# Kernel tuning notes

Measured on AMD Instinct MI355X. Metric: run time of the kernel, lower is better.

Reference implementation:

```python
import jax, jax.numpy as jnp
import numpy as np

N, E, D_IN, D, HEADS = 8192, 2048, 256, 256, 4
EPS = 1e-5
NEG = -1e9  # large negative instead of -inf (rows guaranteed non-empty anyway)


def _layernorm(x, g, b):
    mu = jnp.mean(x, axis=-1, keepdims=True)
    var = jnp.mean(jnp.square(x - mu), axis=-1, keepdims=True)
    return (x - mu) * jax.lax.rsqrt(var + EPS) * g + b


def _mha(q_x, kv_x, in_w, in_b, out_w, out_b, mask):
    """torch nn.MultiheadAttention (batch=1, eval) with boolean attn_mask.
    q_x: [Lq, D], kv_x: [Lk, D], mask: [Lq, Lk] True = blocked."""
    hd = D // HEADS
    wq, wk, wv = jnp.split(in_w, 3, axis=0)   # each [D, D]
    bq, bk, bv = jnp.split(in_b, 3, axis=0)
    q = (q_x @ wq.T + bq).reshape(-1, HEADS, hd).transpose(1, 0, 2)  # [h, Lq, hd]
    k = (kv_x @ wk.T + bk).reshape(-1, HEADS, hd).transpose(1, 0, 2)
    v = (kv_x @ wv.T + bv).reshape(-1, HEADS, hd).transpose(1, 0, 2)
    scores = jnp.einsum('hqd,hkd->hqk', q, k) / jnp.sqrt(jnp.asarray(hd, q.dtype))
    scores = jnp.where(mask[None, :, :], NEG, scores)
    attn = jax.nn.softmax(scores, axis=-1)
    out = jnp.einsum('hqk,hkd->hqd', attn, v)           # [h, Lq, hd]
    out = out.transpose(1, 0, 2).reshape(-1, D)          # [Lq, D]
    return out @ out_w.T + out_b


def setup_inputs() -> dict:
    key = jax.random.key(0)
    ks = jax.random.split(key, 12)
    s = 0.02
    x_0 = jax.random.normal(ks[0], (N, D_IN), jnp.float32)
    x_1 = jax.random.normal(ks[1], (E, D_IN), jnp.float32)
    H = (jax.random.uniform(ks[2], (N, E)) < 0.01).astype(jnp.float32)
    H = H.at[jnp.arange(N), jnp.arange(N) % E].set(1.0)
    return {
        'x_0': x_0, 'x_1': x_1, 'incidence_1': H,
        'node_w': jax.random.normal(ks[3], (D, D_IN), jnp.float32) * s,
        'node_b': jnp.zeros((D,), jnp.float32),
        'edge_w': jax.random.normal(ks[4], (D, D_IN), jnp.float32) * s,
        'edge_b': jnp.zeros((D,), jnp.float32),
        'n2e_in_w': jax.random.normal(ks[5], (3 * D, D), jnp.float32) * s,
        'n2e_in_b': jnp.zeros((3 * D,), jnp.float32),
        'n2e_out_w': jax.random.normal(ks[6], (D, D), jnp.float32) * s,
        'n2e_out_b': jnp.zeros((D,), jnp.float32),
        'e2n_in_w': jax.random.normal(ks[7], (3 * D, D), jnp.float32) * s,
        'e2n_in_b': jnp.zeros((3 * D,), jnp.float32),
        'e2n_out_w': jax.random.normal(ks[8], (D, D), jnp.float32) * s,
        'e2n_out_b': jnp.zeros((D,), jnp.float32),
        'norm1_g': jnp.ones((D,), jnp.float32),
        'norm1_b': jnp.zeros((D,), jnp.float32),
        'norm2_g': jnp.ones((D,), jnp.float32),
        'norm2_b': jnp.zeros((D,), jnp.float32),
    }


def reference(x_0, x_1, incidence_1, node_w, node_b, edge_w, edge_b,
              n2e_in_w, n2e_in_b, n2e_out_w, n2e_out_b,
              e2n_in_w, e2n_in_b, e2n_out_w, e2n_out_b,
              norm1_g, norm1_b, norm2_g, norm2_b):
    H = incidence_1                      # [N, E]
    x_0_p = x_0 @ node_w.T + node_b      # [N, D]
    x_1_p = x_1 @ edge_w.T + edge_b      # [E, D]
    # node -> edge: edges query nodes, mask where H.T == 0
    x_1_u = _mha(x_1_p, x_0_p, n2e_in_w, n2e_in_b, n2e_out_w, n2e_out_b,
                 H.T == 0)
    x_1_u = _layernorm(x_1_p + x_1_u, norm1_g, norm1_b)
    # edge -> node: nodes query updated edges, mask where H == 0
    x_0_u = _mha(x_0_p, x_1_u, e2n_in_w, e2n_in_b, e2n_out_w, e2n_out_b,
                 H == 0)
    x_0_u = _layernorm(x_0_p + x_0_u, norm2_g, norm2_b)
    return (x_0_u, x_1_u)
```

## Files before the change

kernel.cpp:

```cpp
#include <hip/hip_runtime.h>
#include <hip/hip_bf16.h>

using bf16 = __hip_bfloat16;
typedef __attribute__((ext_vector_type(4))) float  f32x4;
typedef __attribute__((ext_vector_type(8))) short  s16x8;

#define QSTRIDE 1040
#define ASTRIDE 520
#define BSTRIDE 2064
#define CMAX 256
#define RMAX 128
#define CSTRIDE 16

struct ConvDesc { const float* src[14]; int dstoff[14]; int cnt[14]; };

__global__ __launch_bounds__(256)
void conv_weights(ConvDesc d, bf16* __restrict__ dst, int* __restrict__ cz, int czn)
{
    const int seg = blockIdx.x >> 6;
    const int blk = blockIdx.x & 63;
    if (seg == 14) {
        for (int i = blk * 256 + threadIdx.x; i < czn; i += 64 * 256)
            cz[i] = 0;
        return;
    }
    const float* __restrict__ s = d.src[seg];
    bf16* __restrict__ o = dst + d.dstoff[seg];
    const int n = d.cnt[seg];
    for (int i = blk * 256 + threadIdx.x; i < n; i += 64 * 256)
        o[i] = __float2bfloat16(s[i]);
}

__global__ __launch_bounds__(256, 2)
void proj_lists(const float* __restrict__ X0, const float* __restrict__ X1,
                const bf16* __restrict__ Wc, const bf16* __restrict__ biasc,
                bf16* __restrict__ outB,
                const float* __restrict__ H, int* __restrict__ col_cnt,
                unsigned short* __restrict__ col_idx, int* __restrict__ row_cnt,
                unsigned short* __restrict__ row_idx)
{
    __shared__ __align__(16) bf16 As[4 * QSTRIDE];
    __shared__ __align__(16) bf16 Bs[4 * QSTRIDE];
    __shared__ int rc;

    const int t = threadIdx.x;

    if (blockIdx.x >= 160) {
        int n = blockIdx.x - 160;
        const float* Hp = H + (size_t)n * 2048 + t * 8;
        f32x4 c0 = *(const f32x4*)Hp;
        f32x4 c1 = *(const f32x4*)(Hp + 4);

        while (n < 8192) {
            const int nn = n + 1024;
            f32x4 p0, p1;
            if (nn < 8192) {
                const float* Hq = H + (size_t)nn * 2048 + t * 8;
                p0 = *(const f32x4*)Hq;
                p1 = *(const f32x4*)(Hq + 4);
            }

            if (t == 0) rc = 0;
            __syncthreads();

            float hv[8];
#pragma unroll
            for (int j = 0; j < 4; j++) { hv[j] = c0[j]; hv[4 + j] = c1[j]; }

#pragma unroll
            for (int j = 0; j < 8; j++) {
                if (hv[j] != 0.f) {
                    const int e = t * 8 + j;
                    const int sr = atomicAdd(&rc, 1);
                    if (sr < RMAX) row_idx[(size_t)n * RMAX + sr] = (unsigned short)e;
                    const int sc = atomicAdd(&col_cnt[e * CSTRIDE], 1);
                    if (sc < CMAX) col_idx[(size_t)e * CMAX + sc] = (unsigned short)n;
                }
            }
            __syncthreads();
            if (t == 0) row_cnt[n] = (rc < RMAX) ? rc : RMAX;

            n = nn; c0 = p0; c1 = p1;
        }
        return;
    }

    const int lane = t & 63;
    const int w    = t >> 6;
    const int wm   = (w >> 1) * 64;
    const int wn   = (w & 1) * 64;
    const int bt   = blockIdx.x >> 1;
    const int tn   = (blockIdx.x & 1) * 128;
    if (bt >= 80) return;

    const float* __restrict__ A = (bt < 64) ? X0 : X1;
    const int arow = (bt < 64) ? bt * 128 : (bt - 64) * 128;
    const bf16* __restrict__ W    = Wc    + ((bt < 64) ? 0 : 65536);
    const bf16* __restrict__ bias = biasc + ((bt < 64) ? 0 : 256);
    const int tm = bt * 128;

    f32x4 acc[4][4];
#pragma unroll
    for (int i = 0; i < 4; i++)
#pragma unroll
        for (int j = 0; j < 4; j++)
#pragma unroll
            for (int r = 0; r < 4; r++) acc[i][j][r] = 0.f;

    const int m0 = t >> 2,         q0 = t & 3;
    const int m1 = (t + 256) >> 2, q1 = (t + 256) & 3;
    const int fq = lane >> 4, fr = lane & 15;

    for (int k0 = 0; k0 < 256; k0 += 32) {
        f32x4 a0l = *(const f32x4*)(A + (size_t)(arow + m0) * 256 + k0 + q0 * 8);
        f32x4 a0h = *(const f32x4*)(A + (size_t)(arow + m0) * 256 + k0 + q0 * 8 + 4);
        f32x4 a1l = *(const f32x4*)(A + (size_t)(arow + m1) * 256 + k0 + q1 * 8);
        f32x4 a1h = *(const f32x4*)(A + (size_t)(arow + m1) * 256 + k0 + q1 * 8 + 4);
        union { s16x8 v; bf16 e[8]; } u0, u1;
#pragma unroll
        for (int j = 0; j < 4; j++) {
            u0.e[j] = __float2bfloat16(a0l[j]); u0.e[4 + j] = __float2bfloat16(a0h[j]);
            u1.e[j] = __float2bfloat16(a1l[j]); u1.e[4 + j] = __float2bfloat16(a1h[j]);
        }
        s16x8 sb0 = *(const s16x8*)(W + (size_t)(tn + m0) * 256 + k0 + q0 * 8);
        s16x8 sb1 = *(const s16x8*)(W + (size_t)(tn + m1) * 256 + k0 + q1 * 8);

        __syncthreads();
        *(s16x8*)&As[q0 * QSTRIDE + m0 * 8] = u0.v;
        *(s16x8*)&As[q1 * QSTRIDE + m1 * 8] = u1.v;
        *(s16x8*)&Bs[q0 * QSTRIDE + m0 * 8] = sb0;
        *(s16x8*)&Bs[q1 * QSTRIDE + m1 * 8] = sb1;
        __syncthreads();

        s16x8 af[4], bfv[4];
#pragma unroll
        for (int i = 0; i < 4; i++) {
            af[i]  = *(const s16x8*)&As[fq * QSTRIDE + (wm + i * 16 + fr) * 8];
            bfv[i] = *(const s16x8*)&Bs[fq * QSTRIDE + (wn + i * 16 + fr) * 8];
        }
#pragma unroll
        for (int i = 0; i < 4; i++)
#pragma unroll
            for (int j = 0; j < 4; j++)
                acc[i][j] = __builtin_amdgcn_mfma_f32_16x16x32_bf16(
                    af[i], bfv[j], acc[i][j], 0, 0, 0);
    }

#pragma unroll
    for (int j = 0; j < 4; j++) {
        const int ncol = tn + wn + j * 16 + fr;
        const float bj = __bfloat162float(bias[ncol]);
#pragma unroll
        for (int i = 0; i < 4; i++)
#pragma unroll
            for (int r = 0; r < 4; r++) {
                const int mrow = tm + wm + i * 16 + fq * 4 + r;
                outB[(size_t)mrow * 256 + ncol] = __float2bfloat16(acc[i][j][r] + bj);
            }
    }
}

__global__ __launch_bounds__(256, 2)
void gemm_dual(const bf16* __restrict__ A0, const bf16* __restrict__ W0,
               const bf16* __restrict__ bias0, bf16* __restrict__ out0,
               int N0, int tiles0, int nblk0,
               const bf16* __restrict__ A1, const bf16* __restrict__ W1,
               const bf16* __restrict__ bias1, bf16* __restrict__ out1,
               int N1, int tiles1)
{
    __shared__ __align__(16) bf16 As[4 * QSTRIDE];
    __shared__ __align__(16) bf16 Bs[4 * QSTRIDE];

    const int t    = threadIdx.x;
    const int lane = t & 63;
    const int w    = t >> 6;
    const int wm   = (w >> 1) * 64;
    const int wn   = (w & 1) * 64;

    const bool second = (blockIdx.x >= (unsigned)nblk0);
    const int  bi     = second ? (blockIdx.x - nblk0) : blockIdx.x;
    const bf16* __restrict__ A    = second ? A1 : A0;
    const bf16* __restrict__ W    = second ? W1 : W0;
    const bf16* __restrict__ bias = second ? bias1 : bias0;
    bf16* __restrict__ outB       = second ? out1 : out0;
    const int N      = second ? N1 : N0;
    const int tilesN = second ? tiles1 : tiles0;
    const int tm = (bi / tilesN) * 128;
    const int tn = (bi % tilesN) * 128;

    f32x4 acc[4][4];
#pragma unroll
    for (int i = 0; i < 4; i++)
#pragma unroll
        for (int j = 0; j < 4; j++)
#pragma unroll
            for (int r = 0; r < 4; r++) acc[i][j][r] = 0.f;

    const int m0 = t >> 2,         q0 = t & 3;
    const int m1 = (t + 256) >> 2, q1 = (t + 256) & 3;
    const int fq = lane >> 4, fr = lane & 15;

    for (int k0 = 0; k0 < 256; k0 += 32) {
        s16x8 sa0 = *(const s16x8*)(A + (size_t)(tm + m0) * 256 + k0 + q0 * 8);
        s16x8 sa1 = *(const s16x8*)(A + (size_t)(tm + m1) * 256 + k0 + q1 * 8);
        s16x8 sb0 = *(const s16x8*)(W + (size_t)(tn + m0) * 256 + k0 + q0 * 8);
        s16x8 sb1 = *(const s16x8*)(W + (size_t)(tn + m1) * 256 + k0 + q1 * 8);

        __syncthreads();
        *(s16x8*)&As[q0 * QSTRIDE + m0 * 8] = sa0;
        *(s16x8*)&As[q1 * QSTRIDE + m1 * 8] = sa1;
        *(s16x8*)&Bs[q0 * QSTRIDE + m0 * 8] = sb0;
        *(s16x8*)&Bs[q1 * QSTRIDE + m1 * 8] = sb1;
        __syncthreads();

        s16x8 af[4], bfv[4];
#pragma unroll
        for (int i = 0; i < 4; i++) {
            af[i]  = *(const s16x8*)&As[fq * QSTRIDE + (wm + i * 16 + fr) * 8];
            bfv[i] = *(const s16x8*)&Bs[fq * QSTRIDE + (wn + i * 16 + fr) * 8];
        }
#pragma unroll
        for (int i = 0; i < 4; i++)
#pragma unroll
            for (int j = 0; j < 4; j++)
                acc[i][j] = __builtin_amdgcn_mfma_f32_16x16x32_bf16(
                    af[i], bfv[j], acc[i][j], 0, 0, 0);
    }

#pragma unroll
    for (int j = 0; j < 4; j++) {
        const int ncol = tn + wn + j * 16 + fr;
        const float bj = __bfloat162float(bias[ncol]);
#pragma unroll
        for (int i = 0; i < 4; i++)
#pragma unroll
            for (int r = 0; r < 4; r++) {
                const int mrow = tm + wm + i * 16 + fq * 4 + r;
                outB[(size_t)mrow * N + ncol] = __float2bfloat16(acc[i][j][r] + bj);
            }
    }
}

__global__ __launch_bounds__(256, 2)
void gemm_ln(const bf16* __restrict__ A, const bf16* __restrict__ W,
             const float* __restrict__ biasF, const bf16* __restrict__ xp,
             const float* __restrict__ g, const float* __restrict__ b,
             float* __restrict__ outF, bf16* __restrict__ outB)
{
    __shared__ __align__(16) bf16 As[4 * ASTRIDE];
    __shared__ __align__(16) bf16 Bs[4 * BSTRIDE];
    __shared__ float rs1[64], rs2[64];

    const int t    = threadIdx.x;
    const int lane = t & 63;
    const int w    = t >> 6;
    const int fq   = lane >> 4;
    const int fr   = lane & 15;
    const int tm   = blockIdx.x * 64;

    if (t < 64) { rs1[t] = 0.f; rs2[t] = 0.f; }

    f32x4 acc[4][4];
#pragma unroll
    for (int i = 0; i < 4; i++)
#pragma unroll
        for (int j = 0; j < 4; j++)
#pragma unroll
            for (int r = 0; r < 4; r++) acc[i][j][r] = 0.f;

    const int mA = t >> 2, qA = t & 3;

    for (int k0 = 0; k0 < 256; k0 += 32) {
        s16x8 sa = *(const s16x8*)(A + (size_t)(tm + mA) * 256 + k0 + qA * 8);
        s16x8 sb[4];
#pragma unroll
        for (int s = 0; s < 4; s++)
            sb[s] = *(const s16x8*)(W + (size_t)(mA + 64 * s) * 256 + k0 + qA * 8);

        __syncthreads();
        *(s16x8*)&As[qA * ASTRIDE + mA * 8] = sa;
#pragma unroll
        for (int s = 0; s < 4; s++)
            *(s16x8*)&Bs[qA * BSTRIDE + (mA + 64 * s) * 8] = sb[s];
        __syncthreads();

        s16x8 af[4], bfv[4];
#pragma unroll
        for (int i = 0; i < 4; i++) {
            af[i]  = *(const s16x8*)&As[fq * ASTRIDE + (i * 16 + fr) * 8];
            bfv[i] = *(const s16x8*)&Bs[fq * BSTRIDE + (w * 64 + i * 16 + fr) * 8];
        }
#pragma unroll
        for (int i = 0; i < 4; i++)
#pragma unroll
            for (int j = 0; j < 4; j++)
                acc[i][j] = __builtin_amdgcn_mfma_f32_16x16x32_bf16(
                    af[i], bfv[j], acc[i][j], 0, 0, 0);
    }

    float bj[4], gj[4], bbj[4];
    int colv[4];
#pragma unroll
    for (int j = 0; j < 4; j++) {
        colv[j] = w * 64 + j * 16 + fr;
        bj[j]  = biasF[colv[j]];
        gj[j]  = g[colv[j]];
        bbj[j] = b[colv[j]];
    }

#pragma unroll
    for (int i = 0; i < 4; i++) {
#pragma unroll
        for (int r = 0; r < 4; r++) {
            const int row = i * 16 + fq * 4 + r;
            float t1 = 0.f, t2 = 0.f;
#pragma unroll
            for (int j = 0; j < 4; j++) {
                float v = acc[i][j][r] + bj[j]
                        + __bfloat162float(xp[(size_t)(tm + row) * 256 + colv[j]]);
                acc[i][j][r] = v;
                t1 += v;
                t2 += v * v;
            }
#pragma unroll
            for (int o = 1; o < 16; o <<= 1) {
                t1 += __shfl_xor(t1, o);
                t2 += __shfl_xor(t2, o);
            }
            if (fr == 0) {
                atomicAdd(&rs1[row], t1);
                atomicAdd(&rs2[row], t2);
            }
        }
    }
    __syncthreads();

#pragma unroll
    for (int i = 0; i < 4; i++) {
#pragma unroll
        for (int r = 0; r < 4; r++) {
            const int row = i * 16 + fq * 4 + r;
            const float mu  = rs1[row] * (1.f / 256.f);
            const float var = rs2[row] * (1.f / 256.f) - mu * mu;
            const float rstd = rsqrtf(var + 1e-5f);
#pragma unroll
            for (int j = 0; j < 4; j++) {
                const float y = (acc[i][j][r] - mu) * rstd * gj[j] + bbj[j];
                outF[(size_t)(tm + row) * 256 + colv[j]] = y;
                if (outB) outB[(size_t)(tm + row) * 256 + colv[j]] = __float2bfloat16(y);
            }
        }
    }
}

__global__ __launch_bounds__(256)
void sparse_attn(const bf16* __restrict__ Q, int qs,
                 const bf16* __restrict__ Kb, const bf16* __restrict__ Vb, int kvs,
                 const int* __restrict__ cnts, int cstride,
                 const unsigned short* __restrict__ idx,
                 int lmax, int idxmask, bf16* __restrict__ out)
{
    __shared__ float sc[4][CMAX];
    __shared__ unsigned short nls[CMAX];
    const int qi   = blockIdx.x;
    const int h    = threadIdx.x >> 6;
    const int lane = threadIdx.x & 63;
    const int grp  = lane >> 3;
    const int sub  = lane & 7;

    int n = cnts[(size_t)qi * cstride];
    if (n > lmax) n = lmax;

    if (h == 0)
        for (int i = lane; i < n; i += 64)
            nls[i] = (unsigned short)(((int)idx[(size_t)qi * lmax + i]) & idxmask);
    __syncthreads();

    if (n <= 0) {
        out[(size_t)qi * 256 + h * 64 + lane] = __float2bfloat16(0.f);
        return;
    }

    float qv[8];
    {
        union { f32x4 v; unsigned short u[8]; } qu;
        qu.v = *(const f32x4*)(Q + (size_t)qi * qs + h * 64 + sub * 8);
#pragma unroll
        for (int j = 0; j < 8; j++)
            qv[j] = __uint_as_float(((unsigned)qu.u[j]) << 16) * 0.125f;
    }

    float mx = -1e30f;
#pragma unroll 2
    for (int base = 0; base < n; base += 8) {
        const int i = base + grp;
        float s = -1e30f;
        if (i < n) {
            const int nb = nls[i];
            union { f32x4 v; unsigned short u[8]; } ku;
            ku.v = *(const f32x4*)(Kb + (size_t)nb * kvs + h * 64 + sub * 8);
            float a = 0.f;
#pragma unroll
            for (int j = 0; j < 8; j++)
                a += __uint_as_float(((unsigned)ku.u[j]) << 16) * qv[j];
            a += __shfl_xor(a, 1);
            a += __shfl_xor(a, 2);
            a += __shfl_xor(a, 4);
            if (sub == 0) sc[h][i] = a;
            s = a;
        }
        mx = fmaxf(mx, s);
    }
#pragma unroll
    for (int o = 32; o > 0; o >>= 1) mx = fmaxf(mx, __shfl_xor(mx, o));

    float sum = 0.f;
    for (int base = 0; base < n; base += 64) {
        const int i = base + lane;
        if (i < n) {
            const float p = __expf(sc[h][i] - mx);
            sc[h][i] = p;
            sum += p;
        }
    }
#pragma unroll
    for (int o = 32; o > 0; o >>= 1) sum += __shfl_xor(sum, o);
    const float inv = 1.f / sum;

    float oa[8];
#pragma unroll
    for (int j = 0; j < 8; j++) oa[j] = 0.f;
#pragma unroll 2
    for (int base = 0; base < n; base += 8) {
        const int i = base + grp;
        if (i < n) {
            const float p = sc[h][i];
            const int nb = nls[i];
            union { f32x4 v; unsigned short u[8]; } vu;
            vu.v = *(const f32x4*)(Vb + (size_t)nb * kvs + h * 64 + sub * 8);
#pragma unroll
            for (int j = 0; j < 8; j++)
                oa[j] += p * __uint_as_float(((unsigned)vu.u[j]) << 16);
        }
    }
#pragma unroll
    for (int j = 0; j < 8; j++) {
        oa[j] += __shfl_xor(oa[j], 8);
        oa[j] += __shfl_xor(oa[j], 16);
        oa[j] += __shfl_xor(oa[j], 32);
    }
    if (grp == 0) {
        union { s16x8 v; bf16 e[8]; } ou;
#pragma unroll
        for (int j = 0; j < 8; j++) ou.e[j] = __float2bfloat16(oa[j] * inv);
        *(s16x8*)(out + (size_t)qi * 256 + h * 64 + sub * 8) = ou.v;
    }
}

extern "C" void kernel_launch(void* const* d_in, const int* in_sizes, int n_in,
                              void* d_out, int out_size, void* d_ws, size_t ws_size,
                              hipStream_t stream)
{
    const int N = 8192, E = 2048;

    float* out0 = (float*)d_out;
    float* out1 = (float*)d_out + (size_t)N * 256;

    char* wp = (char*)d_ws;
    auto carve = [&](size_t bytes) { void* p = wp; wp += (bytes + 15) & ~size_t(15); return p; };

    bf16*  wcat    = (bf16*)          carve(657408 * 2);
    int*   col_cnt = (int*)           carve((size_t)E * CSTRIDE * 4);
    int*   row_cnt = (int*)           carve((size_t)N * 4);
    unsigned short* col_idx = (unsigned short*)carve((size_t)E * CMAX * 2);
    unsigned short* row_idx = (unsigned short*)carve((size_t)N * RMAX * 2);
    bf16*  xp01    = (bf16*) carve((size_t)(N + E) * 256 * 2);
    bf16*  kvq     = (bf16*) carve((size_t)N * 768 * 2);
    bf16*  q1      = (bf16*) carve((size_t)E * 256 * 2);
    bf16*  attn1   = (bf16*) carve((size_t)E * 256 * 2);
    bf16*  x1u_b   = (bf16*) carve((size_t)E * 256 * 2);
    bf16*  kv2     = (bf16*) carve((size_t)E * 512 * 2);
    bf16*  attn2   = (bf16*) carve((size_t)N * 256 * 2);

    bf16* x0p = xp01;
    bf16* x1p = xp01 + (size_t)N * 256;

    const int O_PW   = 0;
    const int O_PB   = 131072;
    const int O_KVQ  = 131584;
    const int O_KVQB = 328192;
    const int O_Q1W  = 328960;
    const int O_Q1B  = 394496;
    const int O_KV2W = 394752;
    const int O_KV2B = 525824;
    const int O_O1W  = 526336;
    const int O_O2W  = 591872;

    ConvDesc cd;
    const float* srcs[14] = {
        (const float*)d_in[3], (const float*)d_in[5],
        (const float*)d_in[4], (const float*)d_in[6],
        (const float*)d_in[7] + 65536, (const float*)d_in[11],
        (const float*)d_in[8] + 256,   (const float*)d_in[12],
        (const float*)d_in[7],         (const float*)d_in[8],
        (const float*)d_in[11] + 65536,(const float*)d_in[12] + 256,
        (const float*)d_in[9],         (const float*)d_in[13]
    };
    const int offs[14] = {O_PW, O_PW + 65536, O_PB, O_PB + 256,
                          O_KVQ, O_KVQ + 131072, O_KVQB, O_KVQB + 512,
                          O_Q1W, O_Q1B, O_KV2W, O_KV2B, O_O1W, O_O2W};
    const int cnts[14] = {65536, 65536, 256, 256, 131072, 65536, 512, 256,
                          65536, 256, 131072, 512, 65536, 65536};
    for (int i = 0; i < 14; i++) { cd.src[i] = srcs[i]; cd.dstoff[i] = offs[i]; cd.cnt[i] = cnts[i]; }

    conv_weights<<<15 * 64, 256, 0, stream>>>(cd, wcat, col_cnt, E * CSTRIDE);

    proj_lists<<<160 + 1024, 256, 0, stream>>>(
        (const float*)d_in[0], (const float*)d_in[1],
        wcat + O_PW, wcat + O_PB, xp01,
        (const float*)d_in[2], col_cnt, col_idx, row_cnt, row_idx);

    gemm_dual<<<384 + 32, 256, 0, stream>>>(x0p, wcat + O_KVQ, wcat + O_KVQB, kvq,
                                            768, 6, 384,
                                            x1p, wcat + O_Q1W, wcat + O_Q1B, q1,
                                            256, 2);

    sparse_attn<<<E, 256, 0, stream>>>(q1, 256, kvq, kvq + 256, 768,
                                       col_cnt, CSTRIDE, col_idx, CMAX, N - 1, attn1);
    gemm_ln<<<E / 64, 256, 0, stream>>>(attn1, wcat + O_O1W, (const float*)d_in[10],
                                        x1p, (const float*)d_in[15], (const float*)d_in[16],
                                        out1, x1u_b);

    gemm_dual<<<64, 256, 0, stream>>>(x1u_b, wcat + O_KV2W, wcat + O_KV2B, kv2,
                                      512, 4, 64,
                                      nullptr, nullptr, nullptr, nullptr, 256, 2);
    sparse_attn<<<N, 256, 0, stream>>>(kvq + 512, 768, kv2, kv2 + 256, 512,
                                       row_cnt, 1, row_idx, RMAX, E - 1, attn2);
    gemm_ln<<<N / 64, 256, 0, stream>>>(attn2, wcat + O_O2W, (const float*)d_in[14],
                                        x0p, (const float*)d_in[17], (const float*)d_in[18],
                                        out0, nullptr);
}
```

Baseline: 277.1 us.

## Split incidence list building into ballot-based row pass and separate column pass

Moves construction of the sparse row and column lists out of the fused projection kernel into two dedicated kernels. Row lists are built with one wavefront per node, using wave ballots and popcount prefix sums in place of shared-memory atomics and block barriers. Column lists are then built from the compact row lists instead of rescanning the dense incidence matrix. This removes per-element LDS atomics and syncthreads, but adds two extra launches and loses the overlap between the dense H scan and the projection GEMM.

```diff
diff --git a/kernel.cpp b/kernel.cpp
--- a/kernel.cpp
+++ b/kernel.cpp
@@ -31,60 +31,64 @@
         o[i] = __float2bfloat16(s[i]);
 }
 
+__global__ __launch_bounds__(256)
+void build_rows(const float* __restrict__ H, int* __restrict__ row_cnt,
+                unsigned short* __restrict__ row_idx)
+{
+    const int lane = threadIdx.x & 63;
+    const int n    = blockIdx.x * 4 + (threadIdx.x >> 6);
+
+    const unsigned long long ltm = (1ull << lane) - 1ull;
+    int base = 0;
+
+#pragma unroll
+    for (int seg = 0; seg < 8; seg++) {
+        f32x4 v = *(const f32x4*)(H + (size_t)n * 2048 + seg * 256 + lane * 4);
+        unsigned long long b[4];
+#pragma unroll
+        for (int j = 0; j < 4; j++) b[j] = __ballot(v[j] != 0.f);
+
+        int pre = 0;
+#pragma unroll
+        for (int j = 0; j < 4; j++) {
+            if (v[j] != 0.f) {
+                const int slot = base + pre + (int)__popcll(b[j] & ltm);
+                if (slot < RMAX)
+                    row_idx[(size_t)n * RMAX + slot] =
+                        (unsigned short)(seg * 256 + lane * 4 + j);
+            }
+            pre += (int)__popcll(b[j]);
+        }
+        base += pre;
+    }
+    if (lane == 0) row_cnt[n] = (base < RMAX) ? base : RMAX;
+}
+
+__global__ __launch_bounds__(256)
+void build_cols(const int* __restrict__ row_cnt,
+                const unsigned short* __restrict__ row_idx,
+                int* __restrict__ col_cnt, unsigned short* __restrict__ col_idx)
+{
+    const int g = blockIdx.x * 256 + threadIdx.x;
+    const int n = g >> 3;
+    const int t = g & 7;
+    const int cnt = row_cnt[n];
+    for (int i = t; i < cnt; i += 8) {
+        const int e = row_idx[(size_t)n * RMAX + i];
+        const int s = atomicAdd(&col_cnt[e * CSTRIDE], 1);
+        if (s < CMAX) col_idx[(size_t)e * CMAX + s] = (unsigned short)n;
+    }
+}
+
 __global__ __launch_bounds__(256, 2)
-void proj_lists(const float* __restrict__ X0, const float* __restrict__ X1,
-                const bf16* __restrict__ Wc, const bf16* __restrict__ biasc,
-                bf16* __restrict__ outB,
-                const float* __restrict__ H, int* __restrict__ col_cnt,
-                unsigned short* __restrict__ col_idx, int* __restrict__ row_cnt,
-                unsigned short* __restrict__ row_idx)
+void gemm_proj(const float* __restrict__ X0, const float* __restrict__ X1,
+               const bf16* __restrict__ Wc, const bf16* __restrict__ biasc,
+               bf16* __restrict__ outB)
 {
     __shared__ __align__(16) bf16 As[4 * QSTRIDE];
     __shared__ __align__(16) bf16 Bs[4 * QSTRIDE];
-    __shared__ int rc;
-
-    const int t = threadIdx.x;
-
-    if (blockIdx.x >= 160) {
-        int n = blockIdx.x - 160;
-        const float* Hp = H + (size_t)n * 2048 + t * 8;
-        f32x4 c0 = *(const f32x4*)Hp;
-        f32x4 c1 = *(const f32x4*)(Hp + 4);
-
-        while (n < 8192) {
-            const int nn = n + 1024;
-            f32x4 p0, p1;
-            if (nn < 8192) {
-                const float* Hq = H + (size_t)nn * 2048 + t * 8;
-                p0 = *(const f32x4*)Hq;
-                p1 = *(const f32x4*)(Hq + 4);
-            }
-
-            if (t == 0) rc = 0;
-            __syncthreads();
-
-            float hv[8];
-#pragma unroll
-            for (int j = 0; j < 4; j++) { hv[j] = c0[j]; hv[4 + j] = c1[j]; }
-
-#pragma unroll
-            for (int j = 0; j < 8; j++) {
-                if (hv[j] != 0.f) {
-                    const int e = t * 8 + j;
-                    const int sr = atomicAdd(&rc, 1);
-                    if (sr < RMAX) row_idx[(size_t)n * RMAX + sr] = (unsigned short)e;
-                    const int sc = atomicAdd(&col_cnt[e * CSTRIDE], 1);
-                    if (sc < CMAX) col_idx[(size_t)e * CMAX + sc] = (unsigned short)n;
-                }
-            }
-            __syncthreads();
-            if (t == 0) row_cnt[n] = (rc < RMAX) ? rc : RMAX;
-
-            n = nn; c0 = p0; c1 = p1;
-        }
-        return;
-    }
-
+
+    const int t    = threadIdx.x;
     const int lane = t & 63;
     const int w    = t >> 6;
     const int wm   = (w >> 1) * 64;
@@ -515,10 +519,12 @@
 
     conv_weights<<<15 * 64, 256, 0, stream>>>(cd, wcat, col_cnt, E * CSTRIDE);
 
-    proj_lists<<<160 + 1024, 256, 0, stream>>>(
-        (const float*)d_in[0], (const float*)d_in[1],
-        wcat + O_PW, wcat + O_PB, xp01,
-        (const float*)d_in[2], col_cnt, col_idx, row_cnt, row_idx);
+    build_rows<<<N / 4, 256, 0, stream>>>((const float*)d_in[2], row_cnt, row_idx);
+
+    build_cols<<<N * 8 / 256, 256, 0, stream>>>(row_cnt, row_idx, col_cnt, col_idx);
+
+    gemm_proj<<<160, 256, 0, stream>>>((const float*)d_in[0], (const float*)d_in[1],
+                                       wcat + O_PW, wcat + O_PB, xp01);
 
     gemm_dual<<<384 + 32, 256, 0, stream>>>(x0p, wcat + O_KVQ, wcat + O_KVQB, kvq,
                                             768, 6, 384,
```

Result: faster. 256.4 us (-7.5%).
